# Performance work log

Hardware: AMD Instinct MI355X
Metric: run time of the kernel (lower is better)

## Reference

```python
import jax, jax.numpy as jnp
import numpy as np

B, N, D = 32, 512, 768
L = 2            # gcn_num_layers
NBR = 4          # 4 trait branches
FH, NC = 256, 2  # final_hidden_size, num_classes
GAMMA, ZETA, BETA = -0.1, 1.1, 2.0 / 3.0  # hard-concrete constants


def setup_inputs() -> dict:
    key = jax.random.key(0)
    ks = jax.random.split(key, 8)
    s_in = 1.0 / np.sqrt(D)
    return {
        "pmask": jnp.ones((B, N), jnp.float32),
        "feature": jax.random.normal(ks[0], (B, N, D), jnp.float32),
        "Wq": jax.random.normal(ks[1], (NBR, L, D, D), jnp.float32) * s_in,
        "Wk": jax.random.normal(ks[2], (NBR, L, D, D), jnp.float32) * s_in,
        "proj_w": jax.random.normal(ks[3], (NBR, D), jnp.float32) * s_in,
        "proj_b": jnp.zeros((NBR,), jnp.float32),
        "fc1_w": jax.random.normal(ks[4], (NBR, FH, D), jnp.float32) * s_in,
        "fc1_b": jnp.zeros((NBR, FH), jnp.float32),
        "fc2_w": jax.random.normal(ks[5], (NBR, FH, FH), jnp.float32) * (1.0 / np.sqrt(FH)),
        "fc2_b": jnp.zeros((NBR, FH), jnp.float32),
        "fcf_w": jax.random.normal(ks[6], (NBR, NC, FH), jnp.float32) * (1.0 / np.sqrt(FH)),
        "fcf_b": jnp.zeros((NBR, NC), jnp.float32),
    }


def _l2c(feat, full_adj, wq, wk):
    """Deterministic hard-concrete pairwise sparsifier -> (adj, l0_loss)."""
    q = jnp.einsum("bnd,de->bne", feat, wq)
    k = jnp.einsum("bnd,de->bne", feat, wk)
    logits = jnp.einsum("bqd,bkd->bqk", q, k) / np.sqrt(D)
    gate = jnp.clip(jax.nn.sigmoid(logits) * (ZETA - GAMMA) + GAMMA, 0.0, 1.0)
    adj = gate * full_adj
    p_open = jax.nn.sigmoid(logits - BETA * np.log(-GAMMA / ZETA))
    l0 = jnp.sum(p_open * full_adj) / jnp.maximum(jnp.sum(full_adj), 1.0)
    return adj, l0


def _deeper_gcn(pmask, feature, wq_l, wk_l, pw, pb):
    full_adj = pmask[:, :, None] * pmask[:, None, :]  # [B,N,N]
    feat = feature
    preds = [feat]
    l0_total = 0.0
    for l in range(L):
        adj, l0 = _l2c(feat, full_adj, wq_l[l], wk_l[l])
        l0_total = l0_total + l0
        deg = adj.sum(2)                                   # [B,N]
        dis = jnp.where(deg > 0, jnp.where(deg > 0, deg, 1.0) ** -0.5, 0.0)
        dis = jax.lax.stop_gradient(dis)
        adj_n = dis[:, :, None] * adj * dis[:, None, :]    # D^-1/2 A D^-1/2
        feat = jnp.einsum("bij,bid->bjd", adj_n, feat)     # adj_.T @ feat
        preds.append(feat)
    pps = jnp.stack(preds, axis=2)                         # [B,N,L+1,D]
    retain = jax.nn.sigmoid(jnp.einsum("bnld,d->bnl", pps, pw) + pb)[..., None]
    out = (retain * pps).sum(axis=2)                       # [B,N,D]
    return out, l0_total / L


def reference(pmask, feature, Wq, Wk, proj_w, proj_b,
              fc1_w, fc1_b, fc2_w, fc2_b, fcf_w, fcf_b):
    logits_all = []
    for i in range(NBR):
        out, _l0 = _deeper_gcn(pmask, feature, Wq[i], Wk[i], proj_w[i], proj_b[i])
        x = out[:, -1]                                     # context node readout
        h = jax.nn.relu(jnp.einsum("bd,hd->bh", x, fc1_w[i]) + fc1_b[i])
        h = jax.nn.relu(jnp.einsum("bh,gh->bg", h, fc2_w[i]) + fc2_b[i])
        logits_all.append(jnp.einsum("bg,cg->bc", h, fcf_w[i]) + fcf_b[i])
    return jnp.stack(logits_all, axis=1)                   # [B,4,NC]
```

## Files before the change

kernel.cpp:

```cpp
#include <hip/hip_runtime.h>
#include <hip/hip_bf16.h>
#include <math.h>

#define B_ 32
#define N_ 512
#define D_ 768
#define L_ 2
#define NBR_ 4
#define FH_ 256
#define NC_ 2

typedef __attribute__((ext_vector_type(8))) short short8;
typedef __attribute__((ext_vector_type(4))) short short4v;
typedef __attribute__((ext_vector_type(4))) float f32x4;

static constexpr float kInvSqrtD = 0.03608439182435161f;

__device__ __forceinline__ void gl2lds16(const void* g, void* l) {
  __builtin_amdgcn_global_load_lds(
      (const __attribute__((address_space(1))) unsigned int*)g,
      (__attribute__((address_space(3))) unsigned int*)l, 16, 0, 0);
}
__device__ __forceinline__ unsigned short f2bf(float f) {
  __hip_bfloat16 h = __float2bfloat16(f);
  return *reinterpret_cast<unsigned short*>(&h);
}
__device__ __forceinline__ float bf2f(unsigned short u) {
  unsigned int x = ((unsigned int)u) << 16;
  return __builtin_bit_cast(float, x);
}
__device__ __forceinline__ float deg2dis(float d) {
  return d > 0.0f ? rsqrtf(d) : 0.0f;
}

__device__ __forceinline__ void nt_gemm_core(
    const unsigned short* __restrict__ A, const unsigned short* __restrict__ BT,
    int K, int bm, int bn, short* As, short* Bs, f32x4 (&acc)[4][4]) {
  const int tid = threadIdx.x;
  const int lane = tid & 63;
  const int w = tid >> 6, wr = w >> 1, wc = w & 1;
  const int srow = tid >> 2;
  const int scol = (tid & 3) * 8;
  const int kb = lane >> 4;
  const int fr = lane & 15;
  for (int k0 = 0; k0 < K; k0 += 32) {
    gl2lds16(A + (size_t)(bm + srow) * K + k0 + scol, As + tid * 8);
    gl2lds16(A + (size_t)(bm + 64 + srow) * K + k0 + scol, As + 2048 + tid * 8);
    gl2lds16(BT + (size_t)(bn + srow) * K + k0 + scol, Bs + tid * 8);
    gl2lds16(BT + (size_t)(bn + 64 + srow) * K + k0 + scol, Bs + 2048 + tid * 8);
    __syncthreads();
    short8 a[4], b[4];
#pragma unroll
    for (int m = 0; m < 4; ++m)
      a[m] = *reinterpret_cast<const short8*>(&As[(wr * 64 + m * 16 + fr) * 32 + kb * 8]);
#pragma unroll
    for (int n = 0; n < 4; ++n)
      b[n] = *reinterpret_cast<const short8*>(&Bs[(wc * 64 + n * 16 + fr) * 32 + kb * 8]);
#pragma unroll
    for (int m = 0; m < 4; ++m)
#pragma unroll
      for (int n = 0; n < 4; ++n)
        acc[m][n] = __builtin_amdgcn_mfma_f32_16x16x32_bf16(a[m], b[n], acc[m][n], 0, 0, 0);
    __syncthreads();
  }
}

__global__ __launch_bounds__(256) void mt_kernel(
    const __hip_bfloat16* __restrict__ Wkbf, const __hip_bfloat16* __restrict__ Wqbf,
    __hip_bfloat16* __restrict__ MT) {
  __shared__ short As[4096], Bs[4096];
  const size_t zoff = (size_t)blockIdx.z * D_ * D_;
  const unsigned short* A = (const unsigned short*)Wkbf + zoff;
  const unsigned short* BT = (const unsigned short*)Wqbf + zoff;
  unsigned short* Out = (unsigned short*)MT + zoff;
  const int bm = blockIdx.x * 128, bn = blockIdx.y * 128;
  f32x4 acc[4][4] = {};
  nt_gemm_core(A, BT, D_, bm, bn, As, Bs, acc);
  const int lane = threadIdx.x & 63, w = threadIdx.x >> 6;
  const int wr = w >> 1, wc = w & 1, kb = lane >> 4, fr = lane & 15;
#pragma unroll
  for (int m = 0; m < 4; ++m)
#pragma unroll
    for (int n = 0; n < 4; ++n)
#pragma unroll
      for (int r = 0; r < 4; ++r) {
        int row = bm + wr * 64 + m * 16 + kb * 4 + r;
        int col = bn + wc * 64 + n * 16 + fr;
        Out[(size_t)row * D_ + col] = f2bf(acc[m][n][r]);
      }
}

__global__ __launch_bounds__(256) void p_kernel(
    const __hip_bfloat16* __restrict__ feat, const __hip_bfloat16* __restrict__ MT,
    __hip_bfloat16* __restrict__ P, float* __restrict__ deg) {
  __shared__ short As[4096], Bs[4096];
  if (blockIdx.y == 0 && blockIdx.x < 64) {
    deg[blockIdx.x * 256 + threadIdx.x] = 0.0f;
  }
  const unsigned short* A = (const unsigned short*)feat;
  const unsigned short* BT = (const unsigned short*)MT;
  unsigned short* Out = (unsigned short*)P;
  const int bm = blockIdx.x * 128, bn = blockIdx.y * 128;
  f32x4 acc[4][4] = {};
  nt_gemm_core(A, BT, D_, bm, bn, As, Bs, acc);
  const int lane = threadIdx.x & 63, w = threadIdx.x >> 6;
  const int wr = w >> 1, wc = w & 1, kb = lane >> 4, fr = lane & 15;
#pragma unroll
  for (int m = 0; m < 4; ++m)
#pragma unroll
    for (int n = 0; n < 4; ++n)
#pragma unroll
      for (int r = 0; r < 4; ++r) {
        int row = bm + wr * 64 + m * 16 + kb * 4 + r;
        int col = bn + wc * 64 + n * 16 + fr;
        Out[(size_t)row * D_ + col] = f2bf(acc[m][n][r]);
      }
}

template <bool WFULL>
__global__ __launch_bounds__(256) void logits_kernel(
    const __hip_bfloat16* __restrict__ feat, const __hip_bfloat16* __restrict__ P,
    const float* __restrict__ pmask, __hip_bfloat16* __restrict__ GT,
    float* __restrict__ deg) {
  __shared__ short As[4096], Bs[4096];
  const int b = blockIdx.z;
  const unsigned short* A = (const unsigned short*)feat + (size_t)b * N_ * D_;
  const unsigned short* BT = (const unsigned short*)P + (size_t)b * N_ * D_;
  unsigned short* G = (unsigned short*)GT + (size_t)b * N_ * N_;
  const int bm = blockIdx.x * 128, bn = blockIdx.y * 128;
  f32x4 acc[4][4] = {};
  nt_gemm_core(A, BT, D_, bm, bn, As, Bs, acc);
  const int lane = threadIdx.x & 63, w = threadIdx.x >> 6;
  const int wr = w >> 1, wc = w & 1, kb = lane >> 4, fr = lane & 15;
  float colsum[4] = {0.f, 0.f, 0.f, 0.f};
#pragma unroll
  for (int m = 0; m < 4; ++m) {
    float pk[4];
#pragma unroll
    for (int r = 0; r < 4; ++r)
      pk[r] = pmask[b * N_ + bm + wr * 64 + m * 16 + kb * 4 + r];
#pragma unroll
    for (int n = 0; n < 4; ++n) {
      int col = bn + wc * 64 + n * 16 + fr;
      float pq = pmask[b * N_ + col];
#pragma unroll
      for (int r = 0; r < 4; ++r) {
        int row = bm + wr * 64 + m * 16 + kb * 4 + r;
        float x = acc[m][n][r] * kInvSqrtD;
        float s = 1.0f / (1.0f + __expf(-x));
        float g = fminf(fmaxf(s * 1.2f - 0.1f, 0.0f), 1.0f);
        float v = g * pk[r] * pq;
        if (WFULL || row >= 384)
          G[(size_t)row * N_ + col] = f2bf(v);
        colsum[n] += v;
      }
    }
  }
#pragma unroll
  for (int n = 0; n < 4; ++n) {
    float s = colsum[n];
    s += __shfl_xor(s, 16, 64);
    s += __shfl_xor(s, 32, 64);
    if (lane < 16)
      atomicAdd(&deg[b * N_ + bn + wc * 64 + n * 16 + fr], s);
  }
}

template <bool WBF>
__global__ __launch_bounds__(256) void agg_kernel(
    const __hip_bfloat16* __restrict__ GT, const __hip_bfloat16* __restrict__ FT,
    const float* __restrict__ deg, float* __restrict__ flast,
    __hip_bfloat16* __restrict__ fbf, int j_off) {
  __shared__ short As[4096], Bs[4096];
  const int b = blockIdx.z;
  const unsigned short* A = (const unsigned short*)GT + (size_t)b * N_ * N_;
  const unsigned short* BT = (const unsigned short*)FT + (size_t)b * D_ * N_;
  const int bm = j_off + blockIdx.x * 128, bn = blockIdx.y * 128;
  f32x4 acc[4][4] = {};
  nt_gemm_core(A, BT, N_, bm, bn, As, Bs, acc);
  const int lane = threadIdx.x & 63, w = threadIdx.x >> 6;
  const int wr = w >> 1, wc = w & 1, kb = lane >> 4, fr = lane & 15;
#pragma unroll
  for (int m = 0; m < 4; ++m) {
#pragma unroll
    for (int r = 0; r < 4; ++r) {
      int row = bm + wr * 64 + m * 16 + kb * 4 + r;
      float dj = deg2dis(deg[b * N_ + row]);
#pragma unroll
      for (int n = 0; n < 4; ++n) {
        int col = bn + wc * 64 + n * 16 + fr;
        float v = acc[m][n][r] * dj;
        if (WBF)
          fbf[((size_t)b * N_ + row) * D_ + col] = __float2bfloat16(v);
        if (row == N_ - 1)
          flast[(size_t)b * D_ + col] = v;
      }
    }
  }
}

__global__ __launch_bounds__(256) void t0_kernel(
    const __hip_bfloat16* __restrict__ feat0, __hip_bfloat16* __restrict__ FT0raw) {
  __shared__ unsigned short Ts[64][68];
  const int b = blockIdx.z;
  const int i0 = blockIdx.x * 64, d0 = blockIdx.y * 64;
  const int t = threadIdx.x;
  const int r16 = t >> 4, c4 = (t & 15) * 4;
  const unsigned short* F = (const unsigned short*)feat0;
  unsigned short* O = (unsigned short*)FT0raw;
#pragma unroll
  for (int p = 0; p < 4; ++p) {
    int i = r16 + p * 16;
    short4v sv = *reinterpret_cast<const short4v*>(&F[((size_t)b * N_ + i0 + i) * D_ + d0 + c4]);
    Ts[i][c4 + 0] = (unsigned short)sv.x; Ts[i][c4 + 1] = (unsigned short)sv.y;
    Ts[i][c4 + 2] = (unsigned short)sv.z; Ts[i][c4 + 3] = (unsigned short)sv.w;
  }
  __syncthreads();
#pragma unroll
  for (int q = 0; q < 4; ++q) {
    int d = r16 + q * 16;
    short4v o;
#pragma unroll
    for (int e = 0; e < 4; ++e) o[e] = (short)Ts[c4 + e][d];
    *reinterpret_cast<short4v*>(&O[((size_t)b * D_ + d0 + d) * N_ + i0 + c4]) = o;
  }
}

__global__ __launch_bounds__(256) void scale_ft_kernel(
    const __hip_bfloat16* __restrict__ FT0raw, const float* __restrict__ deg,
    __hip_bfloat16* __restrict__ FT) {
  const size_t e0 = ((size_t)blockIdx.x * 256 + threadIdx.x) * 8;
  const int b = (int)(e0 / ((size_t)D_ * N_));
  const int i = (int)(e0 % N_);
  const float* dg = deg + b * N_ + i;
  short8 v = *reinterpret_cast<const short8*>((const unsigned short*)FT0raw + e0);
  short8 o;
#pragma unroll
  for (int e = 0; e < 8; ++e)
    o[e] = (short)f2bf(bf2f((unsigned short)v[e]) * deg2dis(dg[e]));
  *reinterpret_cast<short8*>((unsigned short*)FT + e0) = o;
}

__global__ __launch_bounds__(256) void tscale_kernel(
    const __hip_bfloat16* __restrict__ fin, const float* __restrict__ deg,
    __hip_bfloat16* __restrict__ FT) {
  __shared__ float Ts[64][65];
  const int b = blockIdx.z;
  const int i0 = blockIdx.x * 64, d0 = blockIdx.y * 64;
  const int t = threadIdx.x;
  const int r16 = t >> 4, c4 = (t & 15) * 4;
  const unsigned short* F = (const unsigned short*)fin;
#pragma unroll
  for (int p = 0; p < 4; ++p) {
    int i = r16 + p * 16;
    short4v sv = *reinterpret_cast<const short4v*>(&F[((size_t)b * N_ + i0 + i) * D_ + d0 + c4]);
    Ts[i][c4 + 0] = bf2f((unsigned short)sv.x);
    Ts[i][c4 + 1] = bf2f((unsigned short)sv.y);
    Ts[i][c4 + 2] = bf2f((unsigned short)sv.z);
    Ts[i][c4 + 3] = bf2f((unsigned short)sv.w);
  }
  __syncthreads();
#pragma unroll
  for (int q = 0; q < 4; ++q) {
    int d = r16 + q * 16;
    short4v o;
#pragma unroll
    for (int e = 0; e < 4; ++e) {
      float dv = deg2dis(deg[b * N_ + i0 + c4 + e]);
      o[e] = (short)f2bf(Ts[c4 + e][d] * dv);
    }
    *reinterpret_cast<short4v*>((unsigned short*)FT + ((size_t)b * D_ + d0 + d) * N_ + i0 + c4) = o;
  }
}

__global__ __launch_bounds__(256) void cvt_kernel(const float* __restrict__ src,
                                                  __hip_bfloat16* __restrict__ dst) {
  int i = blockIdx.x * 256 + threadIdx.x;
  float4 v = reinterpret_cast<const float4*>(src)[i];
  short4v o = {(short)f2bf(v.x), (short)f2bf(v.y), (short)f2bf(v.z), (short)f2bf(v.w)};
  reinterpret_cast<short4v*>(dst)[i] = o;
}

__global__ __launch_bounds__(256) void head_all_kernel(
    const float* __restrict__ feature, const float* __restrict__ flast1,
    const float* __restrict__ flast2, const float* __restrict__ proj_w,
    const float* __restrict__ proj_b, const float* __restrict__ fc1_w,
    const float* __restrict__ fc1_b, const float* __restrict__ fc2_w,
    const float* __restrict__ fc2_b, const float* __restrict__ fcf_w,
    const float* __restrict__ fcf_b, float* __restrict__ out) {
  const int b = blockIdx.x, br = blockIdx.y;
  __shared__ float p[3][D_];
  __shared__ float x[D_];
  __shared__ float h1[FH_];
  __shared__ float h2[FH_];
  __shared__ float retain[3];
  const int tid = threadIdx.x;
  const float4* f0 = (const float4*)(feature + ((size_t)b * N_ + (N_ - 1)) * D_);
  const float4* f1 = (const float4*)(flast1 + ((size_t)br * B_ + b) * D_);
  const float4* f2 = (const float4*)(flast2 + ((size_t)br * B_ + b) * D_);
  for (int d4 = tid; d4 < D_ / 4; d4 += 256) {
    *reinterpret_cast<float4*>(&p[0][d4 * 4]) = f0[d4];
    *reinterpret_cast<float4*>(&p[1][d4 * 4]) = f1[d4];
    *reinterpret_cast<float4*>(&p[2][d4 * 4]) = f2[d4];
  }
  __syncthreads();
  const int w = tid >> 6, lane = tid & 63;
  const float* pw = proj_w + (size_t)br * D_;
  if (w < 3) {
    float s = 0.0f;
    for (int d = lane; d < D_; d += 64) s += p[w][d] * pw[d];
#pragma unroll
    for (int off = 32; off; off >>= 1) s += __shfl_down(s, off, 64);
    if (lane == 0) retain[w] = 1.0f / (1.0f + __expf(-(s + proj_b[br])));
  }
  __syncthreads();
  for (int d = tid; d < D_; d += 256)
    x[d] = retain[0] * p[0][d] + retain[1] * p[1][d] + retain[2] * p[2][d];
  __syncthreads();
  {
    const float4* w4 = (const float4*)(fc1_w + ((size_t)br * FH_ + tid) * D_);
    const float4* x4 = (const float4*)x;
    float4 a = {0.f, 0.f, 0.f, 0.f};
#pragma unroll 4
    for (int d4 = 0; d4 < D_ / 4; ++d4) {
      float4 wv = w4[d4], xv = x4[d4];
      a.x += wv.x * xv.x; a.y += wv.y * xv.y;
      a.z += wv.z * xv.z; a.w += wv.w * xv.w;
    }
    float s = a.x + a.y + a.z + a.w + fc1_b[br * FH_ + tid];
    h1[tid] = fmaxf(s, 0.0f);
  }
  __syncthreads();
  {
    const float4* w4 = (const float4*)(fc2_w + ((size_t)br * FH_ + tid) * FH_);
    const float4* x4 = (const float4*)h1;
    float4 a = {0.f, 0.f, 0.f, 0.f};
#pragma unroll 4
    for (int d4 = 0; d4 < FH_ / 4; ++d4) {
      float4 wv = w4[d4], xv = x4[d4];
      a.x += wv.x * xv.x; a.y += wv.y * xv.y;
      a.z += wv.z * xv.z; a.w += wv.w * xv.w;
    }
    float s = a.x + a.y + a.z + a.w + fc2_b[br * FH_ + tid];
    h2[tid] = fmaxf(s, 0.0f);
  }
  __syncthreads();
  if (w < NC_) {
    float s = 0.0f;
    for (int g = lane; g < FH_; g += 64) s += h2[g] * fcf_w[((size_t)br * NC_ + w) * FH_ + g];
#pragma unroll
    for (int off = 32; off; off >>= 1) s += __shfl_down(s, off, 64);
    if (lane == 0) out[((size_t)b * NBR_ + br) * NC_ + w] = s + fcf_b[br * NC_ + w];
  }
}

extern "C" void kernel_launch(void* const* d_in, const int* in_sizes, int n_in,
                              void* d_out, int out_size, void* d_ws, size_t ws_size,
                              hipStream_t stream) {
  (void)in_sizes; (void)n_in; (void)out_size; (void)ws_size;
  const float* pmask   = (const float*)d_in[0];
  const float* feature = (const float*)d_in[1];
  const float* Wq      = (const float*)d_in[2];
  const float* Wk      = (const float*)d_in[3];
  const float* proj_w  = (const float*)d_in[4];
  const float* proj_b  = (const float*)d_in[5];
  const float* fc1_w   = (const float*)d_in[6];
  const float* fc1_b   = (const float*)d_in[7];
  const float* fc2_w   = (const float*)d_in[8];
  const float* fc2_b   = (const float*)d_in[9];
  const float* fcf_w   = (const float*)d_in[10];
  const float* fcf_b   = (const float*)d_in[11];
  float* out = (float*)d_out;

  const size_t nBND  = (size_t)B_ * N_ * D_;
  const size_t nW    = (size_t)NBR_ * L_ * D_ * D_;
  const size_t nBNN  = (size_t)B_ * N_ * N_;

  char* p = (char*)d_ws;
  __hip_bfloat16* feat0  = (__hip_bfloat16*)p; p += nBND * 2;
  __hip_bfloat16* Wqbf   = (__hip_bfloat16*)p; p += nW * 2;
  __hip_bfloat16* Wkbf   = (__hip_bfloat16*)p; p += nW * 2;
  __hip_bfloat16* MT     = (__hip_bfloat16*)p; p += nW * 2;
  __hip_bfloat16* Pb     = (__hip_bfloat16*)p; p += nBND * 2;
  __hip_bfloat16* GT     = (__hip_bfloat16*)p; p += nBNN * 2;
  __hip_bfloat16* FT     = (__hip_bfloat16*)p; p += nBND * 2;
  __hip_bfloat16* FT0raw = (__hip_bfloat16*)p; p += nBND * 2;
  __hip_bfloat16* f1bf   = (__hip_bfloat16*)p; p += nBND * 2;
  float* deg    = (float*)p; p += (size_t)B_ * N_ * 4;
  float* flast1 = (float*)p; p += (size_t)NBR_ * B_ * D_ * 4;
  float* flast2 = (float*)p; p += (size_t)NBR_ * B_ * D_ * 4;

  dim3 blk(256);
  cvt_kernel<<<dim3((unsigned)(nBND / 1024)), blk, 0, stream>>>(feature, feat0);
  cvt_kernel<<<dim3((unsigned)(nW / 1024)), blk, 0, stream>>>(Wq, Wqbf);
  cvt_kernel<<<dim3((unsigned)(nW / 1024)), blk, 0, stream>>>(Wk, Wkbf);
  mt_kernel<<<dim3(6, 6, 8), blk, 0, stream>>>(Wkbf, Wqbf, MT);
  t0_kernel<<<dim3(8, 12, B_), blk, 0, stream>>>(feat0, FT0raw);

  for (int i = 0; i < NBR_; ++i) {
    for (int l = 0; l < L_; ++l) {
      const size_t woff = ((size_t)i * L_ + l) * D_ * D_;
      const __hip_bfloat16* featbf = l ? f1bf : feat0;
      p_kernel<<<dim3(128, 6), blk, 0, stream>>>(featbf, MT + woff, Pb, deg);
      if (l == 0) {
        logits_kernel<true><<<dim3(4, 4, 32), blk, 0, stream>>>(featbf, Pb, pmask, GT, deg);
        scale_ft_kernel<<<dim3((unsigned)(nBND / 2048)), blk, 0, stream>>>(FT0raw, deg, FT);
        agg_kernel<true><<<dim3(4, 6, 32), blk, 0, stream>>>(
            GT, FT, deg, flast1 + (size_t)i * B_ * D_, f1bf, 0);
      } else {
        logits_kernel<false><<<dim3(4, 4, 32), blk, 0, stream>>>(featbf, Pb, pmask, GT, deg);
        tscale_kernel<<<dim3(8, 12, 32), blk, 0, stream>>>(f1bf, deg, FT);
        agg_kernel<false><<<dim3(1, 6, 32), blk, 0, stream>>>(
            GT, FT, deg, flast2 + (size_t)i * B_ * D_, nullptr, 384);
      }
    }
  }
  head_all_kernel<<<dim3(B_, NBR_), blk, 0, stream>>>(
      feature, flast1, flast2, proj_w, proj_b, fc1_w, fc1_b, fc2_w, fc2_b,
      fcf_w, fcf_b, out);
}
```

Measured before the change: 920.0 us.

## Batch all four branches into single launches per layer

Adds a branch dimension to the grid of the p, logits, scale, transpose-scale and aggregation kernels so all four trait branches run in one launch per stage instead of four sequential launches. Per-branch buffers (P/FT, GT, f1, deg) are allocated when workspace allows, with a fallback to the old sequential loop otherwise. The aim is to fill the GPU better on small grids such as the 1x6x32 aggregation and to cut launch count, at the price of roughly four times the workspace footprint. The head kernel also moves to 1024 threads, splitting each fc dot product across four lanes.

```diff
diff --git a/kernel.cpp b/kernel.cpp
--- a/kernel.cpp
+++ b/kernel.cpp
@@ -9,6 +9,10 @@
 #define NBR_ 4
 #define FH_ 256
 #define NC_ 2
+#define BN_   ((size_t)B_ * N_)
+#define NBND_ ((size_t)B_ * N_ * D_)
+#define NBNN_ ((size_t)B_ * N_ * N_)
+#define NW_   ((size_t)NBR_ * L_ * D_ * D_)
 
 typedef __attribute__((ext_vector_type(8))) short short8;
 typedef __attribute__((ext_vector_type(4))) short short4v;
@@ -91,15 +95,16 @@
 }
 
 __global__ __launch_bounds__(256) void p_kernel(
-    const __hip_bfloat16* __restrict__ feat, const __hip_bfloat16* __restrict__ MT,
+    const __hip_bfloat16* __restrict__ feat, size_t a_br_stride,
+    const __hip_bfloat16* __restrict__ MTl, size_t mt_br_stride,
     __hip_bfloat16* __restrict__ P, float* __restrict__ deg) {
   __shared__ short As[4096], Bs[4096];
-  if (blockIdx.y == 0 && blockIdx.x < 64) {
-    deg[blockIdx.x * 256 + threadIdx.x] = 0.0f;
-  }
-  const unsigned short* A = (const unsigned short*)feat;
-  const unsigned short* BT = (const unsigned short*)MT;
-  unsigned short* Out = (unsigned short*)P;
+  const int br = blockIdx.z;
+  if (blockIdx.y == 0 && blockIdx.x < 64)
+    deg[br * BN_ + blockIdx.x * 256 + threadIdx.x] = 0.0f;
+  const unsigned short* A = (const unsigned short*)feat + (size_t)br * a_br_stride;
+  const unsigned short* BT = (const unsigned short*)MTl + (size_t)br * mt_br_stride;
+  unsigned short* Out = (unsigned short*)P + (size_t)br * NBND_;
   const int bm = blockIdx.x * 128, bn = blockIdx.y * 128;
   f32x4 acc[4][4] = {};
   nt_gemm_core(A, BT, D_, bm, bn, As, Bs, acc);
@@ -119,14 +124,15 @@
 
 template <bool WFULL>
 __global__ __launch_bounds__(256) void logits_kernel(
-    const __hip_bfloat16* __restrict__ feat, const __hip_bfloat16* __restrict__ P,
-    const float* __restrict__ pmask, __hip_bfloat16* __restrict__ GT,
-    float* __restrict__ deg) {
+    const __hip_bfloat16* __restrict__ feat, size_t a_br_stride,
+    const __hip_bfloat16* __restrict__ P, const float* __restrict__ pmask,
+    __hip_bfloat16* __restrict__ GT, float* __restrict__ deg) {
   __shared__ short As[4096], Bs[4096];
-  const int b = blockIdx.z;
-  const unsigned short* A = (const unsigned short*)feat + (size_t)b * N_ * D_;
-  const unsigned short* BT = (const unsigned short*)P + (size_t)b * N_ * D_;
-  unsigned short* G = (unsigned short*)GT + (size_t)b * N_ * N_;
+  const int br = blockIdx.z >> 5, b = blockIdx.z & 31;
+  const unsigned short* A = (const unsigned short*)feat + (size_t)br * a_br_stride + (size_t)b * N_ * D_;
+  const unsigned short* BT = (const unsigned short*)P + (size_t)br * NBND_ + (size_t)b * N_ * D_;
+  unsigned short* G = (unsigned short*)GT + (size_t)br * NBNN_ + (size_t)b * N_ * N_;
+  float* degb = deg + br * BN_ + b * N_;
   const int bm = blockIdx.x * 128, bn = blockIdx.y * 128;
   f32x4 acc[4][4] = {};
   nt_gemm_core(A, BT, D_, bm, bn, As, Bs, acc);
@@ -162,7 +168,7 @@
     s += __shfl_xor(s, 16, 64);
     s += __shfl_xor(s, 32, 64);
     if (lane < 16)
-      atomicAdd(&deg[b * N_ + bn + wc * 64 + n * 16 + fr], s);
+      atomicAdd(&degb[bn + wc * 64 + n * 16 + fr], s);
   }
 }
 
@@ -172,9 +178,10 @@
     const float* __restrict__ deg, float* __restrict__ flast,
     __hip_bfloat16* __restrict__ fbf, int j_off) {
   __shared__ short As[4096], Bs[4096];
-  const int b = blockIdx.z;
-  const unsigned short* A = (const unsigned short*)GT + (size_t)b * N_ * N_;
-  const unsigned short* BT = (const unsigned short*)FT + (size_t)b * D_ * N_;
+  const int br = blockIdx.z >> 5, b = blockIdx.z & 31;
+  const unsigned short* A = (const unsigned short*)GT + (size_t)br * NBNN_ + (size_t)b * N_ * N_;
+  const unsigned short* BT = (const unsigned short*)FT + (size_t)br * NBND_ + (size_t)b * D_ * N_;
+  const float* degb = deg + br * BN_ + b * N_;
   const int bm = j_off + blockIdx.x * 128, bn = blockIdx.y * 128;
   f32x4 acc[4][4] = {};
   nt_gemm_core(A, BT, N_, bm, bn, As, Bs, acc);
@@ -185,15 +192,15 @@
 #pragma unroll
     for (int r = 0; r < 4; ++r) {
       int row = bm + wr * 64 + m * 16 + kb * 4 + r;
-      float dj = deg2dis(deg[b * N_ + row]);
+      float dj = deg2dis(degb[row]);
 #pragma unroll
       for (int n = 0; n < 4; ++n) {
         int col = bn + wc * 64 + n * 16 + fr;
         float v = acc[m][n][r] * dj;
         if (WBF)
-          fbf[((size_t)b * N_ + row) * D_ + col] = __float2bfloat16(v);
+          fbf[(size_t)br * NBND_ + ((size_t)b * N_ + row) * D_ + col] = __float2bfloat16(v);
         if (row == N_ - 1)
-          flast[(size_t)b * D_ + col] = v;
+          flast[((size_t)br * B_ + b) * D_ + col] = v;
       }
     }
   }
@@ -229,27 +236,28 @@
 __global__ __launch_bounds__(256) void scale_ft_kernel(
     const __hip_bfloat16* __restrict__ FT0raw, const float* __restrict__ deg,
     __hip_bfloat16* __restrict__ FT) {
+  const int br = blockIdx.y;
   const size_t e0 = ((size_t)blockIdx.x * 256 + threadIdx.x) * 8;
   const int b = (int)(e0 / ((size_t)D_ * N_));
   const int i = (int)(e0 % N_);
-  const float* dg = deg + b * N_ + i;
+  const float* dg = deg + br * BN_ + b * N_ + i;
   short8 v = *reinterpret_cast<const short8*>((const unsigned short*)FT0raw + e0);
   short8 o;
 #pragma unroll
   for (int e = 0; e < 8; ++e)
     o[e] = (short)f2bf(bf2f((unsigned short)v[e]) * deg2dis(dg[e]));
-  *reinterpret_cast<short8*>((unsigned short*)FT + e0) = o;
+  *reinterpret_cast<short8*>((unsigned short*)FT + (size_t)br * NBND_ + e0) = o;
 }
 
 __global__ __launch_bounds__(256) void tscale_kernel(
     const __hip_bfloat16* __restrict__ fin, const float* __restrict__ deg,
     __hip_bfloat16* __restrict__ FT) {
   __shared__ float Ts[64][65];
-  const int b = blockIdx.z;
+  const int br = blockIdx.z >> 5, b = blockIdx.z & 31;
   const int i0 = blockIdx.x * 64, d0 = blockIdx.y * 64;
   const int t = threadIdx.x;
   const int r16 = t >> 4, c4 = (t & 15) * 4;
-  const unsigned short* F = (const unsigned short*)fin;
+  const unsigned short* F = (const unsigned short*)fin + (size_t)br * NBND_;
 #pragma unroll
   for (int p = 0; p < 4; ++p) {
     int i = r16 + p * 16;
@@ -266,10 +274,11 @@
     short4v o;
 #pragma unroll
     for (int e = 0; e < 4; ++e) {
-      float dv = deg2dis(deg[b * N_ + i0 + c4 + e]);
+      float dv = deg2dis(deg[br * BN_ + b * N_ + i0 + c4 + e]);
       o[e] = (short)f2bf(Ts[c4 + e][d] * dv);
     }
-    *reinterpret_cast<short4v*>((unsigned short*)FT + ((size_t)b * D_ + d0 + d) * N_ + i0 + c4) = o;
+    *reinterpret_cast<short4v*>((unsigned short*)FT + (size_t)br * NBND_ +
+                                ((size_t)b * D_ + d0 + d) * N_ + i0 + c4) = o;
   }
 }
 
@@ -281,7 +290,7 @@
   reinterpret_cast<short4v*>(dst)[i] = o;
 }
 
-__global__ __launch_bounds__(256) void head_all_kernel(
+__global__ __launch_bounds__(1024) void head_all_kernel(
     const float* __restrict__ feature, const float* __restrict__ flast1,
     const float* __restrict__ flast2, const float* __restrict__ proj_w,
     const float* __restrict__ proj_b, const float* __restrict__ fc1_w,
@@ -295,13 +304,13 @@
   __shared__ float h2[FH_];
   __shared__ float retain[3];
   const int tid = threadIdx.x;
-  const float4* f0 = (const float4*)(feature + ((size_t)b * N_ + (N_ - 1)) * D_);
-  const float4* f1 = (const float4*)(flast1 + ((size_t)br * B_ + b) * D_);
-  const float4* f2 = (const float4*)(flast2 + ((size_t)br * B_ + b) * D_);
-  for (int d4 = tid; d4 < D_ / 4; d4 += 256) {
-    *reinterpret_cast<float4*>(&p[0][d4 * 4]) = f0[d4];
-    *reinterpret_cast<float4*>(&p[1][d4 * 4]) = f1[d4];
-    *reinterpret_cast<float4*>(&p[2][d4 * 4]) = f2[d4];
+  const float4* srcs[3] = {
+      (const float4*)(feature + ((size_t)b * N_ + (N_ - 1)) * D_),
+      (const float4*)(flast1 + ((size_t)br * B_ + b) * D_),
+      (const float4*)(flast2 + ((size_t)br * B_ + b) * D_)};
+  if (tid < 576) {
+    int which = tid / 192, dd = tid % 192;
+    *reinterpret_cast<float4*>(&p[which][dd * 4]) = srcs[which][dd];
   }
   __syncthreads();
   const int w = tid >> 6, lane = tid & 63;
@@ -314,35 +323,41 @@
     if (lane == 0) retain[w] = 1.0f / (1.0f + __expf(-(s + proj_b[br])));
   }
   __syncthreads();
-  for (int d = tid; d < D_; d += 256)
-    x[d] = retain[0] * p[0][d] + retain[1] * p[1][d] + retain[2] * p[2][d];
+  if (tid < D_)
+    x[tid] = retain[0] * p[0][tid] + retain[1] * p[1][tid] + retain[2] * p[2][tid];
   __syncthreads();
   {
-    const float4* w4 = (const float4*)(fc1_w + ((size_t)br * FH_ + tid) * D_);
+    const int outn = tid >> 2, part = tid & 3;
+    const float4* w4 = (const float4*)(fc1_w + ((size_t)br * FH_ + outn) * D_);
     const float4* x4 = (const float4*)x;
     float4 a = {0.f, 0.f, 0.f, 0.f};
 #pragma unroll 4
-    for (int d4 = 0; d4 < D_ / 4; ++d4) {
-      float4 wv = w4[d4], xv = x4[d4];
+    for (int k = part; k < D_ / 4; k += 4) {
+      float4 wv = w4[k], xv = x4[k];
       a.x += wv.x * xv.x; a.y += wv.y * xv.y;
       a.z += wv.z * xv.z; a.w += wv.w * xv.w;
     }
-    float s = a.x + a.y + a.z + a.w + fc1_b[br * FH_ + tid];
-    h1[tid] = fmaxf(s, 0.0f);
+    float s = a.x + a.y + a.z + a.w;
+    s += __shfl_xor(s, 1, 64);
+    s += __shfl_xor(s, 2, 64);
+    if (part == 0) h1[outn] = fmaxf(s + fc1_b[br * FH_ + outn], 0.0f);
   }
   __syncthreads();
   {
-    const float4* w4 = (const float4*)(fc2_w + ((size_t)br * FH_ + tid) * FH_);
+    const int outn = tid >> 2, part = tid & 3;
+    const float4* w4 = (const float4*)(fc2_w + ((size_t)br * FH_ + outn) * FH_);
     const float4* x4 = (const float4*)h1;
     float4 a = {0.f, 0.f, 0.f, 0.f};
 #pragma unroll 4
-    for (int d4 = 0; d4 < FH_ / 4; ++d4) {
-      float4 wv = w4[d4], xv = x4[d4];
+    for (int k = part; k < FH_ / 4; k += 4) {
+      float4 wv = w4[k], xv = x4[k];
       a.x += wv.x * xv.x; a.y += wv.y * xv.y;
       a.z += wv.z * xv.z; a.w += wv.w * xv.w;
     }
-    float s = a.x + a.y + a.z + a.w + fc2_b[br * FH_ + tid];
-    h2[tid] = fmaxf(s, 0.0f);
+    float s = a.x + a.y + a.z + a.w;
+    s += __shfl_xor(s, 1, 64);
+    s += __shfl_xor(s, 2, 64);
+    if (part == 0) h2[outn] = fmaxf(s + fc2_b[br * FH_ + outn], 0.0f);
   }
   __syncthreads();
   if (w < NC_) {
@@ -357,7 +372,7 @@
 extern "C" void kernel_launch(void* const* d_in, const int* in_sizes, int n_in,
                               void* d_out, int out_size, void* d_ws, size_t ws_size,
                               hipStream_t stream) {
-  (void)in_sizes; (void)n_in; (void)out_size; (void)ws_size;
+  (void)in_sizes; (void)n_in; (void)out_size;
   const float* pmask   = (const float*)d_in[0];
   const float* feature = (const float*)d_in[1];
   const float* Wq      = (const float*)d_in[2];
@@ -372,50 +387,75 @@
   const float* fcf_b   = (const float*)d_in[11];
   float* out = (float*)d_out;
 
-  const size_t nBND  = (size_t)B_ * N_ * D_;
-  const size_t nW    = (size_t)NBR_ * L_ * D_ * D_;
-  const size_t nBNN  = (size_t)B_ * N_ * N_;
-
   char* p = (char*)d_ws;
-  __hip_bfloat16* feat0  = (__hip_bfloat16*)p; p += nBND * 2;
-  __hip_bfloat16* Wqbf   = (__hip_bfloat16*)p; p += nW * 2;
-  __hip_bfloat16* Wkbf   = (__hip_bfloat16*)p; p += nW * 2;
-  __hip_bfloat16* MT     = (__hip_bfloat16*)p; p += nW * 2;
-  __hip_bfloat16* Pb     = (__hip_bfloat16*)p; p += nBND * 2;
-  __hip_bfloat16* GT     = (__hip_bfloat16*)p; p += nBNN * 2;
-  __hip_bfloat16* FT     = (__hip_bfloat16*)p; p += nBND * 2;
-  __hip_bfloat16* FT0raw = (__hip_bfloat16*)p; p += nBND * 2;
-  __hip_bfloat16* f1bf   = (__hip_bfloat16*)p; p += nBND * 2;
-  float* deg    = (float*)p; p += (size_t)B_ * N_ * 4;
-  float* flast1 = (float*)p; p += (size_t)NBR_ * B_ * D_ * 4;
-  float* flast2 = (float*)p; p += (size_t)NBR_ * B_ * D_ * 4;
+  auto take = [&](size_t bytes) {
+    char* q = p; p += (bytes + 255) & ~(size_t)255; return q;
+  };
+  __hip_bfloat16* feat0  = (__hip_bfloat16*)take(NBND_ * 2);
+  __hip_bfloat16* MT     = (__hip_bfloat16*)take(NW_ * 2);
+  __hip_bfloat16* FT0raw = (__hip_bfloat16*)take(NBND_ * 2);
+  float* deg    = (float*)take(NBR_ * BN_ * 4);
+  float* flast1 = (float*)take((size_t)NBR_ * B_ * D_ * 4);
+  float* flast2 = (float*)take((size_t)NBR_ * B_ * D_ * 4);
+  const size_t base_used = (size_t)(p - (char*)d_ws);
+  const size_t perbr = NBND_ * 2 + NBNN_ * 2 + NBND_ * 2 + 3 * 256;
+  const int NB = (ws_size >= base_used + 4 * perbr + 4096) ? 4 : 1;
+  __hip_bfloat16* PbFT = (__hip_bfloat16*)take((size_t)NB * NBND_ * 2);
+  __hip_bfloat16* GT   = (__hip_bfloat16*)take((size_t)NB * NBNN_ * 2);
+  __hip_bfloat16* f1bf = (__hip_bfloat16*)take((size_t)NB * NBND_ * 2);
+  __hip_bfloat16* Wqbf = PbFT;
+  __hip_bfloat16* Wkbf = PbFT + NW_;
 
   dim3 blk(256);
-  cvt_kernel<<<dim3((unsigned)(nBND / 1024)), blk, 0, stream>>>(feature, feat0);
-  cvt_kernel<<<dim3((unsigned)(nW / 1024)), blk, 0, stream>>>(Wq, Wqbf);
-  cvt_kernel<<<dim3((unsigned)(nW / 1024)), blk, 0, stream>>>(Wk, Wkbf);
+  cvt_kernel<<<dim3((unsigned)(NBND_ / 1024)), blk, 0, stream>>>(feature, feat0);
+  cvt_kernel<<<dim3((unsigned)(NW_ / 1024)), blk, 0, stream>>>(Wq, Wqbf);
+  cvt_kernel<<<dim3((unsigned)(NW_ / 1024)), blk, 0, stream>>>(Wk, Wkbf);
   mt_kernel<<<dim3(6, 6, 8), blk, 0, stream>>>(Wkbf, Wqbf, MT);
   t0_kernel<<<dim3(8, 12, B_), blk, 0, stream>>>(feat0, FT0raw);
 
-  for (int i = 0; i < NBR_; ++i) {
+  if (NB == 4) {
     for (int l = 0; l < L_; ++l) {
-      const size_t woff = ((size_t)i * L_ + l) * D_ * D_;
-      const __hip_bfloat16* featbf = l ? f1bf : feat0;
-      p_kernel<<<dim3(128, 6), blk, 0, stream>>>(featbf, MT + woff, Pb, deg);
+      const __hip_bfloat16* featA = l ? f1bf : feat0;
+      const size_t astr = l ? NBND_ : 0;
+      p_kernel<<<dim3(128, 6, 4), blk, 0, stream>>>(
+          featA, astr, MT + (size_t)l * D_ * D_, (size_t)L_ * D_ * D_, PbFT, deg);
       if (l == 0) {
-        logits_kernel<true><<<dim3(4, 4, 32), blk, 0, stream>>>(featbf, Pb, pmask, GT, deg);
-        scale_ft_kernel<<<dim3((unsigned)(nBND / 2048)), blk, 0, stream>>>(FT0raw, deg, FT);
-        agg_kernel<true><<<dim3(4, 6, 32), blk, 0, stream>>>(
-            GT, FT, deg, flast1 + (size_t)i * B_ * D_, f1bf, 0);
+        logits_kernel<true><<<dim3(4, 4, 128), blk, 0, stream>>>(
+            featA, astr, PbFT, pmask, GT, deg);
+        scale_ft_kernel<<<dim3(6144, 4), blk, 0, stream>>>(FT0raw, deg, PbFT);
+        agg_kernel<true><<<dim3(4, 6, 128), blk, 0, stream>>>(
+            GT, PbFT, deg, flast1, f1bf, 0);
       } else {
-        logits_kernel<false><<<dim3(4, 4, 32), blk, 0, stream>>>(featbf, Pb, pmask, GT, deg);
-        tscale_kernel<<<dim3(8, 12, 32), blk, 0, stream>>>(f1bf, deg, FT);
-        agg_kernel<false><<<dim3(1, 6, 32), blk, 0, stream>>>(
-            GT, FT, deg, flast2 + (size_t)i * B_ * D_, nullptr, 384);
-      }
-    }
-  }
-  head_all_kernel<<<dim3(B_, NBR_), blk, 0, stream>>>(
+        logits_kernel<false><<<dim3(4, 4, 128), blk, 0, stream>>>(
+            featA, astr, PbFT, pmask, GT, deg);
+        tscale_kernel<<<dim3(8, 12, 128), blk, 0, stream>>>(f1bf, deg, PbFT);
+        agg_kernel<false><<<dim3(1, 6, 128), blk, 0, stream>>>(
+            GT, PbFT, deg, flast2, nullptr, 384);
+      }
+    }
+  } else {
+    for (int i = 0; i < NBR_; ++i) {
+      for (int l = 0; l < L_; ++l) {
+        const __hip_bfloat16* featA = l ? f1bf : feat0;
+        const __hip_bfloat16* MTil = MT + ((size_t)i * L_ + l) * D_ * D_;
+        p_kernel<<<dim3(128, 6, 1), blk, 0, stream>>>(featA, 0, MTil, 0, PbFT, deg);
+        if (l == 0) {
+          logits_kernel<true><<<dim3(4, 4, 32), blk, 0, stream>>>(
+              featA, 0, PbFT, pmask, GT, deg);
+          scale_ft_kernel<<<dim3(6144, 1), blk, 0, stream>>>(FT0raw, deg, PbFT);
+          agg_kernel<true><<<dim3(4, 6, 32), blk, 0, stream>>>(
+              GT, PbFT, deg, flast1 + (size_t)i * B_ * D_, f1bf, 0);
+        } else {
+          logits_kernel<false><<<dim3(4, 4, 32), blk, 0, stream>>>(
+              featA, 0, PbFT, pmask, GT, deg);
+          tscale_kernel<<<dim3(8, 12, 32), blk, 0, stream>>>(f1bf, deg, PbFT);
+          agg_kernel<false><<<dim3(1, 6, 32), blk, 0, stream>>>(
+              GT, PbFT, deg, flast2 + (size_t)i * B_ * D_, nullptr, 384);
+        }
+      }
+    }
+  }
+  head_all_kernel<<<dim3(B_, NBR_), dim3(1024), 0, stream>>>(
       feature, flast1, flast2, proj_w, proj_b, fc1_w, fc1_b, fc2_w, fc2_b,
       fcf_w, fcf_b, out);
 }
```

Result: no change. 914.1 us (-0.6%).
